# Performance work log

Hardware: AMD Instinct MI355X
Metric: run time of the kernel (lower is better)

Reference implementation:

```python
import jax, jax.numpy as jnp
import numpy as np

IMG_W, IMG_H, STRIDE = 640, 360, 32
S = 72
FMAP_H, FMAP_W = IMG_H // STRIDE, IMG_W // STRIDE  # 11, 20
C_IN, C_AF = 512, 64
B, T = 8, 4
LEFT = [72., 60., 49., 39., 30., 22.]
RIGHT = [108., 120., 131., 141., 150., 158.]
BOTTOM = [165., 150., 141., 131., 120., 108., 100., 90., 80., 72., 60., 49., 39., 30., 15.]


def _side_anchors(angles, nb, ys, x=None, y=None):
    # replicates LaneATT generate_side_anchors / generate_anchor, vectorized
    if x is not None:
        sx = np.full(nb, x, np.float64); sy = np.linspace(1., 0., nb)
    else:
        sx = np.linspace(1., 0., nb); sy = np.full(nb, y, np.float64)
    t = np.tan(np.deg2rad(np.asarray(angles, np.float64)))  # [J]
    # xs[i,j,s] = (sx_i + (1 - ys_s - 1 + sy_i)/tan(angle_j)) * img_w
    xs = (sx[:, None, None] + (1. - ys[None, None, :] - 1. + sy[:, None, None]) / t[None, :, None]) * IMG_W
    n = nb * len(angles)
    A = np.zeros((n, 5 + len(ys)), np.float32)
    A[:, 2] = np.repeat(1. - sy, len(angles))
    A[:, 3] = np.repeat(sx, len(angles))
    A[:, 5:] = xs.reshape(n, len(ys)).astype(np.float32)
    return A


def _gen_anchors(ys):
    left = _side_anchors(LEFT, 72, ys, x=0.)
    right = _side_anchors(RIGHT, 72, ys, x=1.)
    bottom = _side_anchors(BOTTOM, 128, ys, y=1.)
    return np.concatenate([left, bottom, right], axis=0)


def setup_inputs() -> dict:
    key = jax.random.key(0)
    ks = jax.random.split(key, 10)
    anchors = _gen_anchors(np.linspace(1., 0., S))            # [A, 77]
    anchors_cut = _gen_anchors(np.linspace(1., 0., FMAP_H))   # [A, 16]
    A = anchors.shape[0]  # 2784
    # compute_anchor_cut_indices
    unclamped = np.flip(np.round(anchors_cut[:, 5:] / STRIDE), axis=1).astype(np.int32)  # [A, H]
    cut_xs = np.clip(unclamped, 0, FMAP_W - 1)
    invalid_mask = (unclamped < 0) | (unclamped > FMAP_W)
    D = C_AF * FMAP_H  # 704
    head_in = (T + 1) * D  # (time_window_size+1)*anchor_feat_channels*fmap_h = 3520
    inp = {
        'x': jax.random.normal(ks[0], (B, T, C_IN, FMAP_H, FMAP_W), jnp.float32),
        'conv1_w': jax.random.normal(ks[1], (C_AF, C_IN), jnp.float32) * 0.02,
        'conv1_b': jnp.zeros((C_AF,), jnp.float32),
        'att_w': jax.random.normal(ks[2], (D, A - 1), jnp.float32) * 0.001,
        'att_b': jnp.zeros((A - 1,), jnp.float32),
        'cls_w': jax.random.normal(ks[3], (head_in, 2), jnp.float32) * 0.001,
        'cls_b': jnp.zeros((2,), jnp.float32),
        'reg_w': jax.random.normal(ks[4], (head_in, S + 2), jnp.float32) * 0.001,
        'reg_b': jnp.zeros((S + 2,), jnp.float32),
        'anchors': jnp.asarray(anchors),
        'cut_xs': jnp.asarray(cut_xs),
        'invalid_mask': jnp.asarray(invalid_mask),
    }
    return inp


def reference(x, conv1_w, conv1_b, att_w, att_b, cls_w, cls_b, reg_w, reg_b,
              anchors, cut_xs, invalid_mask):
    B_, T_, _, H, W = x.shape
    A = anchors.shape[0]
    # conv1: 1x1 conv over backbone features
    feats = jnp.einsum('btchw,oc->btohw', x, conv1_w) + conv1_b[None, None, :, None, None]
    # cut_anchor_features: gather rois[b,t,c,a,h] = feats[b,t,c,h,cut_xs[a,h]]
    Hy = jnp.broadcast_to(jnp.arange(H), cut_xs.shape)       # [A, H]
    rois = feats[:, :, :, Hy, cut_xs]                        # [B, T, C_af, A, H]
    rois = jnp.where(invalid_mask[None, None, None], 0.0, rois)
    rois = jnp.transpose(rois, (0, 1, 3, 2, 4))              # [B, T, A, C_af, H]
    C_af = rois.shape[3]
    D = C_af * H
    past = rois[:, :-1].reshape(B_, T_ - 1, A, D)            # [B, T-1, A, D]
    cur = rois[:, -1].reshape(B_, A, D)                      # [B, A, D]
    # attention_mechanism: softmax scores scattered into off-diagonal of [A, A]
    scores = cur.reshape(B_ * A, D) @ att_w + att_b          # [B*A, A-1]
    att = jax.nn.softmax(scores, axis=1).reshape(B_, A, A - 1)
    j = jnp.arange(A)
    i = j[:, None]
    # column j of row i maps to source index j - (j>i); diagonal is zero
    k = jnp.minimum(jnp.where(j[None, :] > i, j[None, :] - 1, j[None, :]), A - 2)
    Ibd = jnp.broadcast_to(i, (A, A))
    M = jnp.where(jnp.eye(A, dtype=bool)[None], 0.0, att[:, Ibd, k])  # [B, A, A]
    att_feat = jnp.einsum('bia,bad->bid', M, cur)            # [B, A, D]
    # head input: [past frames | attention features | current frame]
    past_p = jnp.transpose(past, (0, 2, 1, 3)).reshape(B_ * A, (T_ - 1) * D)
    head_in = jnp.concatenate([past_p, att_feat.reshape(B_ * A, D), cur.reshape(B_ * A, D)], axis=1)
    cls = (head_in @ cls_w + cls_b).reshape(B_, A, 2)
    reg = (head_in @ reg_w + reg_b).reshape(B_, A, -1)       # [B, A, n_offsets+2]
    base = jnp.broadcast_to(anchors[None], (B_, A, anchors.shape[1]))
    # reg_proposals: [:, :, :2]=cls ; [:, :, 2] from anchor ; [:, :, 3:] = anchor + reg
    reg_proposals = jnp.concatenate([cls, base[..., 2:3], base[..., 3:] + reg], axis=-1)
    return reg_proposals  # [B, A, 5 + n_offsets]
```

## Files before the change

### kernel.cpp

```cpp
#include <hip/hip_runtime.h>

#define BB 8
#define TT 4
#define CIN 512
#define CAF 64
#define HH 11
#define WW 20
#define PP 220
#define PPAD 256
#define AREAL 2784
#define AP 2816
#define DD 704
#define NH 80
#define NHP 128
#define KH 3520
#define NATT 2783

typedef __attribute__((ext_vector_type(8))) short bf16x8;
typedef __attribute__((ext_vector_type(4))) float floatx4;

__device__ __forceinline__ short f2bf(float f) {
  unsigned u = __float_as_uint(f);
  u += 0x7fffu + ((u >> 16) & 1u);
  return (short)(u >> 16);
}
__device__ __forceinline__ float bf2f(short s) {
  return __uint_as_float(((unsigned)(unsigned short)s) << 16);
}

__device__ __forceinline__ void gload_lds16(const void* g, void* l) {
  __builtin_amdgcn_global_load_lds(
      (const __attribute__((address_space(1))) void*)g,
      (__attribute__((address_space(3))) void*)l, 16, 0, 0);
}

__global__ __launch_bounds__(256)
void transpose_x_kernel(const float* __restrict__ x, short* __restrict__ xT)
{
  int bt = blockIdx.x;
  int c0 = blockIdx.y * 32;
  __shared__ float xs[32 * PP];
  int tid = threadIdx.x;
  const float* xp = x + ((long)bt * CIN + c0) * PP;
  for (int i = tid; i < 32 * PP; i += 256) xs[i] = xp[i];
  __syncthreads();
  short* op = xT + (long)bt * PPAD * CIN + c0;
  for (int j = tid; j < PPAD * 32; j += 256) {
    int p = j >> 5, cc = j & 31;
    short v = 0;
    if (p < PP) v = f2bf(xs[cc * PP + p]);
    op[(long)p * CIN + cc] = v;
  }
}

__global__ void prep_wbf_kernel(const float* __restrict__ w, short* __restrict__ wb)
{
  int idx = blockIdx.x * 256 + threadIdx.x;
  if (idx >= 128 * CIN) return;
  int n = idx >> 9, c = idx & 511;
  wb[idx] = (n < CAF) ? f2bf(w[(long)n * CIN + c]) : (short)0;
}

__global__ __launch_bounds__(256)
void gather_cur_kernel(const short* __restrict__ fpo_base, const int* __restrict__ cut_xs,
                       const int* __restrict__ invalid, short* __restrict__ curR)
{
  int g = blockIdx.y;
  int idx = blockIdx.x * 256 + threadIdx.x;
  int a = idx / 88;
  int ch = idx - a * 88;
  int d0 = ch * 8;
  bf16x8 v = {};
  if (a < AREAL) {
    const short* fp = fpo_base + ((long)g * TT + 3) * PPAD * 128;
    #pragma unroll
    for (int e = 0; e < 8; ++e) {
      int d = d0 + e;
      int o = d / 11;
      int hh = d - o * 11;
      int xw = cut_xs[a * 11 + hh];
      v[e] = invalid[a * 11 + hh] ? (short)0 : fp[(hh * 20 + xw) * 128 + o];
    }
  }
  *(bf16x8*)(curR + ((long)g * AP + a) * DD + d0) = v;
}

__global__ __launch_bounds__(256)
void gather_past_kernel(const short* __restrict__ fpo_base, const int* __restrict__ cut_xs,
                        const int* __restrict__ invalid, short* __restrict__ pastR)
{
  int ty = blockIdx.y;
  int g = ty / 3, t = ty - g * 3;
  int idx = blockIdx.x * 256 + threadIdx.x;
  int a = idx / 88;
  int ch = idx - a * 88;
  int d0 = ch * 8;
  bf16x8 v = {};
  if (a < AREAL) {
    const short* fp = fpo_base + ((long)g * TT + t) * PPAD * 128;
    #pragma unroll
    for (int e = 0; e < 8; ++e) {
      int d = d0 + e;
      int o = d / 11;
      int hh = d - o * 11;
      int xw = cut_xs[a * 11 + hh];
      v[e] = invalid[a * 11 + hh] ? (short)0 : fp[(hh * 20 + xw) * 128 + o];
    }
  }
  *(bf16x8*)(pastR + ((long)ty * AP + a) * DD + d0) = v;
}

__global__ __launch_bounds__(256)
void prep_attw_kernel(const float* __restrict__ att_w, short* __restrict__ attwT)
{
  int n0 = blockIdx.x * 32;
  int d0 = blockIdx.y * 32;
  __shared__ float tile[32][33];
  int tid = threadIdx.x;
  for (int i = tid; i < 1024; i += 256) {
    int r = i >> 5, c = i & 31;
    int d = d0 + r, n = n0 + c;
    tile[r][c] = (d < DD && n < NATT) ? att_w[(long)d * NATT + n] : 0.f;
  }
  __syncthreads();
  for (int i = tid; i < 1024; i += 256) {
    int r = i >> 5, c = i & 31;
    attwT[(long)(n0 + r) * DD + d0 + c] = f2bf(tile[c][r]);
  }
}

__global__ void prep_headw_kernel(const float* __restrict__ cls_w, const float* __restrict__ reg_w,
                                  short* __restrict__ headwT)
{
  long idx = (long)blockIdx.x * 256 + threadIdx.x;
  if (idx >= (long)NHP * KH) return;
  int n = (int)(idx / KH), k = (int)(idx % KH);
  float v = 0.f;
  if (n < 2) v = cls_w[(long)k * 2 + n];
  else if (n < 76) v = reg_w[(long)k * 74 + (n - 2)];
  headwT[idx] = f2bf(v);
}

__global__ __launch_bounds__(512, 2)
void gemm256_nt_kernel(const short* __restrict__ A, long long aBatch, int lda,
                       const short* __restrict__ Bt, long long bBatch, int ldb,
                       short* __restrict__ C, long long cBatch, int ldc,
                       int K, const float* __restrict__ bias, int biasN)
{
  int gx = gridDim.x, gy = gridDim.y;
  int nwg = gx * gy * gridDim.z;
  int o = blockIdx.x + gx * (blockIdx.y + gy * blockIdx.z);
  int xcd = o & 7, pos = o >> 3;
  int q = nwg >> 3, r = nwg & 7;
  int nid = (xcd < r ? xcd * (q + 1) : r * (q + 1) + (xcd - r) * q) + pos;
  int bx = nid % gx; int tq = nid / gx; int by = tq % gy; int bz = tq / gy;

  A  += (long long)bz * aBatch;
  Bt += (long long)bz * bBatch;
  C  += (long long)bz * cBatch;
  int M0 = by * 256, N0 = bx * 256;

  __shared__ short lds_a[2 * 256 * 64];
  __shared__ short lds_b[2 * 256 * 64];

  int tid = threadIdx.x, lane = tid & 63, w = tid >> 6;
  int wr = w >> 2, wc = w & 3;

  floatx4 acc[8][4];
  #pragma unroll
  for (int m = 0; m < 8; ++m)
    #pragma unroll
    for (int n = 0; n < 4; ++n) acc[m][n] = floatx4{0.f, 0.f, 0.f, 0.f};

  int rl = tid >> 3, sl = tid & 7;
  int ssl = sl ^ (rl & 7);
  const short* aS = A  + (long)(M0 + rl) * lda + ssl * 8;
  const short* bS = Bt + (long)(N0 + rl) * ldb + ssl * 8;
  char* la0 = (char*)lds_a;
  char* lb0 = (char*)lds_b;
  int wub = (tid & ~63) * 16;

  auto stage = [&](int kt, int buf) {
    long ko = (long)kt * 64;
    #pragma unroll
    for (int c = 0; c < 4; ++c) {
      gload_lds16(aS + (long)c * 64 * lda + ko, la0 + buf * 32768 + c * 8192 + wub);
      gload_lds16(bS + (long)c * 64 * ldb + ko, lb0 + buf * 32768 + c * 8192 + wub);
    }
  };
  auto rdA = [&](int buf, int mf, int kk) -> bf16x8 {
    int row = wr * 128 + mf * 16 + (lane & 15);
    int phys = (kk * 4 + (lane >> 4)) ^ (lane & 7);
    return *(const bf16x8*)(la0 + buf * 32768 + row * 128 + phys * 16);
  };
  auto rdB = [&](int buf, int nf, int kk) -> bf16x8 {
    int row = wc * 64 + nf * 16 + (lane & 15);
    int phys = (kk * 4 + (lane >> 4)) ^ (lane & 7);
    return *(const bf16x8*)(lb0 + buf * 32768 + row * 128 + phys * 16);
  };

  int nt = K >> 6;
  stage(0, 0);
  stage(1, 1);
  asm volatile("s_waitcnt vmcnt(8)" ::: "memory");
  __builtin_amdgcn_sched_barrier(0);
  __builtin_amdgcn_s_barrier();
  __builtin_amdgcn_sched_barrier(0);

  for (int t = 0; t < nt; ++t) {
    int buf = t & 1;
    bf16x8 A0[2][4], A1[2][4], B0[2][2], B1[2][2];
    #pragma unroll
    for (int kk = 0; kk < 2; ++kk) {
      #pragma unroll
      for (int i = 0; i < 4; ++i) A0[kk][i] = rdA(buf, i, kk);
      #pragma unroll
      for (int j = 0; j < 2; ++j) B0[kk][j] = rdB(buf, j, kk);
    }
    __builtin_amdgcn_s_setprio(1);
    #pragma unroll
    for (int kk = 0; kk < 2; ++kk)
      #pragma unroll
      for (int i = 0; i < 4; ++i)
        #pragma unroll
        for (int j = 0; j < 2; ++j)
          acc[i][j] = __builtin_amdgcn_mfma_f32_16x16x32_bf16(A0[kk][i], B0[kk][j], acc[i][j], 0, 0, 0);
    __builtin_amdgcn_s_setprio(0);
    #pragma unroll
    for (int kk = 0; kk < 2; ++kk)
      #pragma unroll
      for (int j = 0; j < 2; ++j) B1[kk][j] = rdB(buf, 2 + j, kk);
    __builtin_amdgcn_s_setprio(1);
    #pragma unroll
    for (int kk = 0; kk < 2; ++kk)
      #pragma unroll
      for (int i = 0; i < 4; ++i)
        #pragma unroll
        for (int j = 0; j < 2; ++j)
          acc[i][2 + j] = __builtin_amdgcn_mfma_f32_16x16x32_bf16(A0[kk][i], B1[kk][j], acc[i][2 + j], 0, 0, 0);
    __builtin_amdgcn_s_setprio(0);
    #pragma unroll
    for (int kk = 0; kk < 2; ++kk)
      #pragma unroll
      for (int i = 0; i < 4; ++i) A1[kk][i] = rdA(buf, 4 + i, kk);
    __builtin_amdgcn_s_setprio(1);
    #pragma unroll
    for (int kk = 0; kk < 2; ++kk)
      #pragma unroll
      for (int i = 0; i < 4; ++i)
        #pragma unroll
        for (int j = 0; j < 2; ++j)
          acc[4 + i][2 + j] = __builtin_amdgcn_mfma_f32_16x16x32_bf16(A1[kk][i], B1[kk][j], acc[4 + i][2 + j], 0, 0, 0);
    __builtin_amdgcn_s_setprio(0);
    __builtin_amdgcn_sched_barrier(0);
    __builtin_amdgcn_s_barrier();
    __builtin_amdgcn_sched_barrier(0);
    if (t + 2 < nt) stage(t + 2, buf);
    __builtin_amdgcn_s_setprio(1);
    #pragma unroll
    for (int kk = 0; kk < 2; ++kk)
      #pragma unroll
      for (int i = 0; i < 4; ++i)
        #pragma unroll
        for (int j = 0; j < 2; ++j)
          acc[4 + i][j] = __builtin_amdgcn_mfma_f32_16x16x32_bf16(A1[kk][i], B0[kk][j], acc[4 + i][j], 0, 0, 0);
    __builtin_amdgcn_s_setprio(0);
    if (t + 2 < nt) {
      asm volatile("s_waitcnt vmcnt(8)" ::: "memory");
    } else {
      asm volatile("s_waitcnt vmcnt(0)" ::: "memory");
    }
    __builtin_amdgcn_sched_barrier(0);
    __builtin_amdgcn_s_barrier();
    __builtin_amdgcn_sched_barrier(0);
  }

  #pragma unroll
  for (int mf = 0; mf < 8; ++mf) {
    #pragma unroll
    for (int nf = 0; nf < 4; ++nf) {
      int col = N0 + wc * 64 + nf * 16 + (lane & 15);
      float bv = 0.f;
      if (bias) bv = (col < biasN) ? bias[col] : 0.f;
      #pragma unroll
      for (int rr = 0; rr < 4; ++rr) {
        int rowc = M0 + wr * 128 + mf * 16 + (lane >> 4) * 4 + rr;
        C[(long)rowc * ldc + col] = f2bf(acc[mf][nf][rr] + bv);
      }
    }
  }
}

template<int WITH_BIAS>
__global__ __launch_bounds__(256)
void gemm_nt_kernel(const short* __restrict__ A, long long aBatch, int lda,
                    const short* __restrict__ Bt, long long bBatch, int ldb,
                    short* __restrict__ C, long long cBatch, int ldc,
                    int K, const float* __restrict__ bias, int biasN)
{
  int gx = gridDim.x, gy = gridDim.y;
  int nwg = gx * gy * gridDim.z;
  int o = blockIdx.x + gx * (blockIdx.y + gy * blockIdx.z);
  int xcd = o & 7, pos = o >> 3;
  int q = nwg >> 3, r = nwg & 7;
  int nid = (xcd < r ? xcd * (q + 1) : r * (q + 1) + (xcd - r) * q) + pos;
  int bx = nid % gx; int t = nid / gx; int by = t % gy; int bz = t / gy;

  A  += (long long)bz * aBatch;
  Bt += (long long)bz * bBatch;
  C  += (long long)bz * cBatch;
  int m0 = by * 128;
  int n0 = bx * 128;

  __shared__ short lds_a[2 * 128 * 32];
  __shared__ short lds_b[2 * 128 * 32];

  int tid = threadIdx.x;
  int lane = tid & 63;
  int wid = tid >> 6;
  int wr = wid >> 1, wc = wid & 1;
  int row = tid >> 2;
  int slot = tid & 3;

  floatx4 acc[4][4];
  #pragma unroll
  for (int m = 0; m < 4; ++m)
    #pragma unroll
    for (int n = 0; n < 4; ++n) acc[m][n] = floatx4{0.f, 0.f, 0.f, 0.f};

  int wbase = (tid & ~63) * 16;
  int ks0 = slot ^ ((row >> 1) & 3);
  int ks1 = slot ^ (((row + 64) >> 1) & 3);
  const short* ar0 = A  + (long)(m0 + row) * lda + ks0 * 8;
  const short* ar1 = A  + (long)(m0 + row + 64) * lda + ks1 * 8;
  const short* br0 = Bt + (long)(n0 + row) * ldb + ks0 * 8;
  const short* br1 = Bt + (long)(n0 + row + 64) * ldb + ks1 * 8;

  auto stage = [&](int kt, int buf) {
    int k0 = kt * 32;
    char* la = (char*)lds_a + buf * 8192 + wbase;
    char* lb = (char*)lds_b + buf * 8192 + wbase;
    gload_lds16(ar0 + k0, la);
    gload_lds16(ar1 + k0, la + 4096);
    gload_lds16(br0 + k0, lb);
    gload_lds16(br1 + k0, lb + 4096);
  };

  int nk = K >> 5;
  stage(0, 0);
  __syncthreads();
  int cur = 0;
  for (int kt = 0; kt < nk; ++kt) {
    if (kt + 1 < nk) stage(kt + 1, cur ^ 1);
    const char* ba = (const char*)lds_a + cur * 8192;
    const char* bb = (const char*)lds_b + cur * 8192;
    bf16x8 af[4], bfv[4];
    #pragma unroll
    for (int m = 0; m < 4; ++m) {
      int rw = wr * 64 + m * 16 + (lane & 15);
      int pp = (lane >> 4) ^ ((rw >> 1) & 3);
      af[m] = *(const bf16x8*)(ba + rw * 64 + (pp << 4));
    }
    #pragma unroll
    for (int n = 0; n < 4; ++n) {
      int rw = wc * 64 + n * 16 + (lane & 15);
      int pp = (lane >> 4) ^ ((rw >> 1) & 3);
      bfv[n] = *(const bf16x8*)(bb + rw * 64 + (pp << 4));
    }
    #pragma unroll
    for (int m = 0; m < 4; ++m)
      #pragma unroll
      for (int n = 0; n < 4; ++n)
        acc[m][n] = __builtin_amdgcn_mfma_f32_16x16x32_bf16(af[m], bfv[n], acc[m][n], 0, 0, 0);
    __syncthreads();
    cur ^= 1;
  }

  #pragma unroll
  for (int m = 0; m < 4; ++m) {
    #pragma unroll
    for (int n = 0; n < 4; ++n) {
      int col = n0 + wc * 64 + n * 16 + (lane & 15);
      float bv = 0.f;
      if (WITH_BIAS) bv = (col < biasN) ? bias[col] : 0.f;
      #pragma unroll
      for (int rr = 0; rr < 4; ++rr) {
        int rowc = m0 + wr * 64 + m * 16 + (lane >> 4) * 4 + rr;
        C[(long)rowc * ldc + col] = f2bf(acc[m][n][rr] + bv);
      }
    }
  }
}

__global__ __launch_bounds__(256)
void softmax_shift_kernel(short* __restrict__ scores)
{
  int g = blockIdx.y;
  int i = blockIdx.x;
  short* row = scores + (long)g * AP * AP + (long)i * AP;
  __shared__ float vals[NATT];
  __shared__ float red[4];
  int tid = threadIdx.x;

  float lmax = -1e30f;
  for (int jc = tid; jc < 348; jc += 256) {
    bf16x8 v8 = *(const bf16x8*)(row + jc * 8);
    #pragma unroll
    for (int e = 0; e < 8; ++e) {
      int j = jc * 8 + e;
      float f = bf2f(v8[e]);
      if (j < NATT) { vals[j] = f; lmax = fmaxf(lmax, f); }
    }
  }
  #pragma unroll
  for (int off = 32; off; off >>= 1) lmax = fmaxf(lmax, __shfl_down(lmax, off, 64));
  if ((tid & 63) == 0) red[tid >> 6] = lmax;
  __syncthreads();
  float mx = fmaxf(fmaxf(red[0], red[1]), fmaxf(red[2], red[3]));
  __syncthreads();

  float lsum = 0.f;
  for (int j = tid; j < NATT; j += 256) {
    float e = __expf(vals[j] - mx);
    vals[j] = e;
    lsum += e;
  }
  #pragma unroll
  for (int off = 32; off; off >>= 1) lsum += __shfl_down(lsum, off, 64);
  if ((tid & 63) == 0) red[tid >> 6] = lsum;
  __syncthreads();
  float inv = 1.f / (red[0] + red[1] + red[2] + red[3]);
  __syncthreads();

  for (int jc = tid; jc < 352; jc += 256) {
    bf16x8 o8;
    #pragma unroll
    for (int e = 0; e < 8; ++e) {
      int j = jc * 8 + e;
      float v;
      if (j < i)            v = vals[j] * inv;
      else if (j == i)      v = 0.f;
      else if (j < AREAL)   v = vals[j - 1] * inv;
      else                  v = 0.f;
      o8[e] = f2bf(v);
    }
    *(bf16x8*)(row + jc * 8) = o8;
  }
}

__device__ __forceinline__
void gemm_n80_body(const short* __restrict__ abase, int ald, int m0,
                   const short* __restrict__ hb, int ldbh,
                   short* __restrict__ lp, int nk,
                   short* lds_a, short* lds_b)
{
  int tid = threadIdx.x, lane = tid & 63, wid = tid >> 6;

  floatx4 acc[2][5];
  #pragma unroll
  for (int m = 0; m < 2; ++m)
    #pragma unroll
    for (int n = 0; n < 5; ++n) acc[m][n] = floatx4{0.f, 0.f, 0.f, 0.f};

  bf16x8 ra[2], rb0, rb1, xa[2], xb0, xb1;
  bool has2 = (tid < 64);

  auto stage_load = [&](int kt, bf16x8* r_a, bf16x8& r_b0, bf16x8& r_b1) {
    int kk = kt * 32;
    #pragma unroll
    for (int it = 0; it < 2; ++it) {
      int rw = it * 64 + (tid >> 2);
      int ks = (tid & 3) ^ ((rw >> 1) & 3);
      r_a[it] = *(const bf16x8*)(abase + (long)(m0 + rw) * ald + kk + ks * 8);
    }
    {
      int n = tid >> 2;
      int ks = (tid & 3) ^ ((n >> 1) & 3);
      r_b0 = *(const bf16x8*)(hb + (long)n * ldbh + kk + ks * 8);
    }
    if (has2) {
      int n = (tid + 256) >> 2;
      int ks = (tid & 3) ^ ((n >> 1) & 3);
      r_b1 = *(const bf16x8*)(hb + (long)n * ldbh + kk + ks * 8);
    }
  };
  auto stage_write = [&](int buf, bf16x8* r_a, bf16x8& r_b0, bf16x8& r_b1) {
    char* la = (char*)lds_a + buf * 8192;
    char* lb = (char*)lds_b + buf * 8192;
    #pragma unroll
    for (int it = 0; it < 2; ++it) {
      int rw = it * 64 + (tid >> 2);
      *(bf16x8*)(la + rw * 64 + ((tid & 3) << 4)) = r_a[it];
    }
    { int n = tid >> 2;
      *(bf16x8*)(lb + n * 64 + ((tid & 3) << 4)) = r_b0; }
    if (has2) {
      int n = (tid + 256) >> 2;
      *(bf16x8*)(lb + n * 64 + ((tid & 3) << 4)) = r_b1;
    }
  };

  stage_load(0, ra, rb0, rb1);
  stage_write(0, ra, rb0, rb1);
  __syncthreads();
  int cur = 0;
  for (int kt = 0; kt < nk; ++kt) {
    bool more = (kt + 1 < nk);
    if (more) stage_load(kt + 1, xa, xb0, xb1);
    const char* la = (const char*)lds_a + cur * 8192;
    const char* lb = (const char*)lds_b + cur * 8192;
    bf16x8 af[2], bfv[5];
    #pragma unroll
    for (int m = 0; m < 2; ++m) {
      int rw = wid * 32 + m * 16 + (lane & 15);
      int pp = (lane >> 4) ^ ((rw >> 1) & 3);
      af[m] = *(const bf16x8*)(la + rw * 64 + (pp << 4));
    }
    #pragma unroll
    for (int n = 0; n < 5; ++n) {
      int nn = n * 16 + (lane & 15);
      int pp = (lane >> 4) ^ ((nn >> 1) & 3);
      bfv[n] = *(const bf16x8*)(lb + nn * 64 + (pp << 4));
    }
    #pragma unroll
    for (int m = 0; m < 2; ++m)
      #pragma unroll
      for (int n = 0; n < 5; ++n)
        acc[m][n] = __builtin_amdgcn_mfma_f32_16x16x32_bf16(af[m], bfv[n], acc[m][n], 0, 0, 0);
    if (more) stage_write(cur ^ 1, xa, xb0, xb1);
    __syncthreads();
    cur ^= 1;
  }

  #pragma unroll
  for (int fm = 0; fm < 2; ++fm)
    #pragma unroll
    for (int fn = 0; fn < 5; ++fn)
      #pragma unroll
      for (int rr = 0; rr < 4; ++rr) {
        int rw = m0 + wid * 32 + fm * 16 + (lane >> 4) * 4 + rr;
        int col = fn * 16 + (lane & 15);
        lp[(long)rw * NH + col] = f2bf(acc[fm][fn][rr]);
      }
}

__global__ __launch_bounds__(256)
void gemm_heads_kernel(const short* __restrict__ pastR, const short* __restrict__ curR,
                       const short* __restrict__ headwT, short* __restrict__ linpart, int G)
{
  int kc = blockIdx.x;
  int m0 = blockIdx.y * 128;
  int g  = blockIdx.z;
  const short* abase;
  const short* hb;
  if (kc == 3) { abase = curR + (long)g * AP * DD; hb = headwT + 4 * DD; }
  else         { abase = pastR + (long)(g * 3 + kc) * AP * DD; hb = headwT + kc * DD; }
  __shared__ short lds_a[2 * 128 * 32];
  __shared__ short lds_b[2 * 128 * 32];
  short* lp = linpart + (long)(kc * G + g) * AP * NH;
  gemm_n80_body(abase, DD, m0, hb, KH, lp, DD / 32, lds_a, lds_b);
}

__global__ __launch_bounds__(256)
void gemm_skinny_kernel(const short* __restrict__ scores, const short* __restrict__ curW3T,
                        short* __restrict__ linpart, int G)
{
  int kc = blockIdx.x;
  int m0 = blockIdx.y * 128;
  int g  = blockIdx.z;
  const short* abase = scores + (long)g * AP * AP + (long)kc * 704;
  const short* hb    = curW3T + (long)g * NHP * AP + (long)kc * 704;
  __shared__ short lds_a[2 * 128 * 32];
  __shared__ short lds_b[2 * 128 * 32];
  short* lp = linpart + (long)((4 + kc) * G + g) * AP * NH;
  gemm_n80_body(abase, AP, m0, hb, AP, lp, 704 / 32, lds_a, lds_b);
}

__global__ void assemble_kernel(const short* __restrict__ linpart, const float* __restrict__ anchors,
                                const float* __restrict__ cls_b, const float* __restrict__ reg_b,
                                float* __restrict__ out_b0, int G)
{
  long idx = (long)blockIdx.x * 256 + threadIdx.x;
  const long per_g = (long)AREAL * 77;
  if (idx >= per_g * G) return;
  int g = (int)(idx / per_g);
  long rem = idx - (long)g * per_g;
  int c = (int)(rem % 77);
  int a = (int)(rem / 77);
  float v;
  if (c == 2) {
    v = anchors[(long)a * 77 + 2];
  } else {
    int col = (c < 2) ? c : (2 + (c - 3));
    float s = 0.f;
    #pragma unroll
    for (int sl = 0; sl < 8; ++sl)
      s += bf2f(linpart[((long)(sl * G + g) * AP + a) * NH + col]);
    v = (c < 2) ? (s + cls_b[c]) : (anchors[(long)a * 77 + c] + s + reg_b[c - 3]);
  }
  out_b0[idx] = v;
}

extern "C" void kernel_launch(void* const* d_in, const int* in_sizes, int n_in,
                              void* d_out, int out_size, void* d_ws, size_t ws_size,
                              hipStream_t stream)
{
  (void)in_sizes; (void)n_in; (void)out_size;
  const float* x        = (const float*)d_in[0];
  const float* conv1_w  = (const float*)d_in[1];
  const float* conv1_b  = (const float*)d_in[2];
  const float* att_w    = (const float*)d_in[3];
  const float* att_b    = (const float*)d_in[4];
  const float* cls_w    = (const float*)d_in[5];
  const float* cls_b    = (const float*)d_in[6];
  const float* reg_w    = (const float*)d_in[7];
  const float* reg_b    = (const float*)d_in[8];
  const float* anchors  = (const float*)d_in[9];
  const int*   cut_xs   = (const int*)d_in[10];
  const int*   invalid  = (const int*)d_in[11];
  float* out = (float*)d_out;

  auto align256 = [](size_t v) { return (v + 255) & ~(size_t)255; };
  const size_t sz_feats  = align256((size_t)BB * TT * PPAD * 128 * 2);
  const size_t sz_wbf    = align256((size_t)128 * CIN * 2);
  const size_t sz_attwT  = align256((size_t)AP * DD * 2);
  const size_t sz_headwT = align256((size_t)NHP * KH * 2);
  const size_t misc = sz_feats + sz_wbf + sz_attwT + sz_headwT;
  auto per_g = [&](int G) {
    return align256((size_t)G * AP * DD * 2)
         + align256((size_t)G * AP * AP * 2)
         + align256((size_t)G * NHP * AP * 2)
         + align256((size_t)8 * G * AP * NH * 2);
  };
  int G = 1;
  for (int cand : {8, 4, 2}) {
    if (misc + per_g(cand) + (1u << 20) <= ws_size) { G = cand; break; }
  }

  char* p = (char*)d_ws;
  short* feats_po = (short*)p; p += sz_feats;
  short* w_bf16   = (short*)p; p += sz_wbf;
  short* attwT    = (short*)p; p += sz_attwT;
  short* headwT   = (short*)p; p += sz_headwT;
  short* curR     = (short*)p; p += align256((size_t)G * AP * DD * 2);
  short* scores   = (short*)p; p += align256((size_t)G * AP * AP * 2);
  short* curW3T   = (short*)p; p += align256((size_t)G * NHP * AP * 2);
  short* linpart  = (short*)p; p += align256((size_t)8 * G * AP * NH * 2);
  short* xT       = scores;
  short* pastR    = scores;

  transpose_x_kernel<<<dim3(BB * TT, CIN / 32), 256, 0, stream>>>(x, xT);
  prep_wbf_kernel<<<(128 * CIN + 255) / 256, 256, 0, stream>>>(conv1_w, w_bf16);
  prep_attw_kernel<<<dim3(AP / 32, DD / 32), 256, 0, stream>>>(att_w, attwT);
  prep_headw_kernel<<<(NHP * KH + 255) / 256, 256, 0, stream>>>(cls_w, reg_w, headwT);

  gemm_nt_kernel<1><<<dim3(1, BB * TT * PPAD / 128, 1), 256, 0, stream>>>(
      xT, 0, CIN, w_bf16, 0, CIN, feats_po, 0, 128, CIN, conv1_b, CAF);

  for (int b0 = 0; b0 < BB; b0 += G) {
    const short* fpo = feats_po + (long)b0 * TT * PPAD * 128;

    gather_cur_kernel<<<dim3(AP * 88 / 256, G), 256, 0, stream>>>(fpo, cut_xs, invalid, curR);

    gemm256_nt_kernel<<<dim3(AP / 256, G * AP / 256, 1), 512, 0, stream>>>(
        curR, 0, DD, attwT, 0, DD, scores, 0, AP, DD, att_b, NATT);

    softmax_shift_kernel<<<dim3(AREAL, G), 256, 0, stream>>>(scores);

    gemm_nt_kernel<0><<<dim3(AP / 128, 1, G), 256, 0, stream>>>(
        headwT + 3 * DD, 0, KH, curR, (long long)AP * DD, DD,
        curW3T, (long long)NHP * AP, AP, DD, nullptr, 0);

    gemm_skinny_kernel<<<dim3(4, AP / 128, G), 256, 0, stream>>>(scores, curW3T, linpart, G);

    gather_past_kernel<<<dim3(AP * 88 / 256, 3 * G), 256, 0, stream>>>(fpo, cut_xs, invalid, pastR);

    gemm_heads_kernel<<<dim3(4, AP / 128, G), 256, 0, stream>>>(pastR, curR, headwT, linpart, G);

    assemble_kernel<<<(int)(((long)G * AREAL * 77 + 255) / 256), 256, 0, stream>>>(
        linpart, anchors, cls_b, reg_b, out + (long)b0 * AREAL * 77, G);
  }
}
```

Measured before the change: 391.1 us.

## Fuse past-frame gather into head GEMM and merge tail GEMMs into one launch

Precomputes a combined gather index table (cut x plus invalid flag) once, so each gathered element needs one index load instead of two. The past-frame gather kernel is removed: the head GEMM now gathers past-frame features straight from the feature map into its A-tile loads, which avoids writing and re-reading the pastR buffer. The skinny attention GEMM and the head GEMMs are merged into a single 8-way launch. In exchange, the fused GEMM does scattered per-element gathers on its A-load path, which may stall the pipeline, and different blocks within one launch now run different code paths.

```diff
diff --git a/kernel.cpp b/kernel.cpp
--- a/kernel.cpp
+++ b/kernel.cpp
@@ -61,9 +61,18 @@
   wb[idx] = (n < CAF) ? f2bf(w[(long)n * CIN + c]) : (short)0;
 }
 
+__global__ void prep_gidx_kernel(const int* __restrict__ cut_xs, const int* __restrict__ invalid,
+                                 int* __restrict__ gidx)
+{
+  int idx = blockIdx.x * 256 + threadIdx.x;
+  if (idx >= AREAL * HH) return;
+  int hh = idx % HH;
+  gidx[idx] = invalid[idx] ? -1 : (hh * WW + cut_xs[idx]) * 128;
+}
+
 __global__ __launch_bounds__(256)
-void gather_cur_kernel(const short* __restrict__ fpo_base, const int* __restrict__ cut_xs,
-                       const int* __restrict__ invalid, short* __restrict__ curR)
+void gather_cur_kernel(const short* __restrict__ fpo_base, const int* __restrict__ gidx,
+                       short* __restrict__ curR)
 {
   int g = blockIdx.y;
   int idx = blockIdx.x * 256 + threadIdx.x;
@@ -78,36 +87,11 @@
       int d = d0 + e;
       int o = d / 11;
       int hh = d - o * 11;
-      int xw = cut_xs[a * 11 + hh];
-      v[e] = invalid[a * 11 + hh] ? (short)0 : fp[(hh * 20 + xw) * 128 + o];
+      int gi = gidx[a * 11 + hh];
+      v[e] = (gi < 0) ? (short)0 : fp[gi + o];
     }
   }
   *(bf16x8*)(curR + ((long)g * AP + a) * DD + d0) = v;
-}
-
-__global__ __launch_bounds__(256)
-void gather_past_kernel(const short* __restrict__ fpo_base, const int* __restrict__ cut_xs,
-                        const int* __restrict__ invalid, short* __restrict__ pastR)
-{
-  int ty = blockIdx.y;
-  int g = ty / 3, t = ty - g * 3;
-  int idx = blockIdx.x * 256 + threadIdx.x;
-  int a = idx / 88;
-  int ch = idx - a * 88;
-  int d0 = ch * 8;
-  bf16x8 v = {};
-  if (a < AREAL) {
-    const short* fp = fpo_base + ((long)g * TT + t) * PPAD * 128;
-    #pragma unroll
-    for (int e = 0; e < 8; ++e) {
-      int d = d0 + e;
-      int o = d / 11;
-      int hh = d - o * 11;
-      int xw = cut_xs[a * 11 + hh];
-      v[e] = invalid[a * 11 + hh] ? (short)0 : fp[(hh * 20 + xw) * 128 + o];
-    }
-  }
-  *(bf16x8*)(pastR + ((long)ty * AP + a) * DD + d0) = v;
 }
 
 __global__ __launch_bounds__(256)
@@ -544,36 +528,141 @@
       }
 }
 
+__device__ __forceinline__
+void gemm_n80_gather_body(const short* __restrict__ fp, const int* __restrict__ gidx,
+                          int m0, const short* __restrict__ hb,
+                          short* __restrict__ lp,
+                          short* lds_a, short* lds_b)
+{
+  int tid = threadIdx.x, lane = tid & 63, wid = tid >> 6;
+
+  floatx4 acc[2][5];
+  #pragma unroll
+  for (int m = 0; m < 2; ++m)
+    #pragma unroll
+    for (int n = 0; n < 5; ++n) acc[m][n] = floatx4{0.f, 0.f, 0.f, 0.f};
+
+  bf16x8 ra[2], rb0, rb1, xa[2], xb0, xb1;
+  bool has2 = (tid < 64);
+
+  auto stage_load = [&](int kt, bf16x8* r_a, bf16x8& r_b0, bf16x8& r_b1) {
+    #pragma unroll
+    for (int it = 0; it < 2; ++it) {
+      int rw = it * 64 + (tid >> 2);
+      int a = m0 + rw;
+      int ks = (tid & 3) ^ ((rw >> 1) & 3);
+      int d0 = kt * 32 + ks * 8;
+      bf16x8 v = {};
+      if (a < AREAL) {
+        #pragma unroll
+        for (int e = 0; e < 8; ++e) {
+          int d = d0 + e;
+          int o = d / 11;
+          int hh = d - o * 11;
+          int gi = gidx[a * 11 + hh];
+          v[e] = (gi < 0) ? (short)0 : fp[gi + o];
+        }
+      }
+      r_a[it] = v;
+    }
+    int kk = kt * 32;
+    {
+      int n = tid >> 2;
+      int ks = (tid & 3) ^ ((n >> 1) & 3);
+      r_b0 = *(const bf16x8*)(hb + (long)n * KH + kk + ks * 8);
+    }
+    if (has2) {
+      int n = (tid + 256) >> 2;
+      int ks = (tid & 3) ^ ((n >> 1) & 3);
+      r_b1 = *(const bf16x8*)(hb + (long)n * KH + kk + ks * 8);
+    }
+  };
+  auto stage_write = [&](int buf, bf16x8* r_a, bf16x8& r_b0, bf16x8& r_b1) {
+    char* la = (char*)lds_a + buf * 8192;
+    char* lb = (char*)lds_b + buf * 8192;
+    #pragma unroll
+    for (int it = 0; it < 2; ++it) {
+      int rw = it * 64 + (tid >> 2);
+      *(bf16x8*)(la + rw * 64 + ((tid & 3) << 4)) = r_a[it];
+    }
+    { int n = tid >> 2;
+      *(bf16x8*)(lb + n * 64 + ((tid & 3) << 4)) = r_b0; }
+    if (has2) {
+      int n = (tid + 256) >> 2;
+      *(bf16x8*)(lb + n * 64 + ((tid & 3) << 4)) = r_b1;
+    }
+  };
+
+  const int nk = 22;
+  stage_load(0, ra, rb0, rb1);
+  stage_write(0, ra, rb0, rb1);
+  __syncthreads();
+  int cur = 0;
+  for (int kt = 0; kt < nk; ++kt) {
+    bool more = (kt + 1 < nk);
+    if (more) stage_load(kt + 1, xa, xb0, xb1);
+    const char* la = (const char*)lds_a + cur * 8192;
+    const char* lb = (const char*)lds_b + cur * 8192;
+    bf16x8 af[2], bfv[5];
+    #pragma unroll
+    for (int m = 0; m < 2; ++m) {
+      int rw = wid * 32 + m * 16 + (lane & 15);
+      int pp = (lane >> 4) ^ ((rw >> 1) & 3);
+      af[m] = *(const bf16x8*)(la + rw * 64 + (pp << 4));
+    }
+    #pragma unroll
+    for (int n = 0; n < 5; ++n) {
+      int nn = n * 16 + (lane & 15);
+      int pp = (lane >> 4) ^ ((nn >> 1) & 3);
+      bfv[n] = *(const bf16x8*)(lb + nn * 64 + (pp << 4));
+    }
+    #pragma unroll
+    for (int m = 0; m < 2; ++m)
+      #pragma unroll
+      for (int n = 0; n < 5; ++n)
+        acc[m][n] = __builtin_amdgcn_mfma_f32_16x16x32_bf16(af[m], bfv[n], acc[m][n], 0, 0, 0);
+    if (more) stage_write(cur ^ 1, xa, xb0, xb1);
+    __syncthreads();
+    cur ^= 1;
+  }
+
+  #pragma unroll
+  for (int fm = 0; fm < 2; ++fm)
+    #pragma unroll
+    for (int fn = 0; fn < 5; ++fn)
+      #pragma unroll
+      for (int rr = 0; rr < 4; ++rr) {
+        int rw = m0 + wid * 32 + fm * 16 + (lane >> 4) * 4 + rr;
+        int col = fn * 16 + (lane & 15);
+        lp[(long)rw * NH + col] = f2bf(acc[fm][fn][rr]);
+      }
+}
+
 __global__ __launch_bounds__(256)
-void gemm_heads_kernel(const short* __restrict__ pastR, const short* __restrict__ curR,
-                       const short* __restrict__ headwT, short* __restrict__ linpart, int G)
+void gemm_tail_kernel(const short* __restrict__ fpo_base, const int* __restrict__ gidx,
+                      const short* __restrict__ curR, const short* __restrict__ scores,
+                      const short* __restrict__ curW3T, const short* __restrict__ headwT,
+                      short* __restrict__ linpart, int G)
 {
   int kc = blockIdx.x;
   int m0 = blockIdx.y * 128;
   int g  = blockIdx.z;
-  const short* abase;
-  const short* hb;
-  if (kc == 3) { abase = curR + (long)g * AP * DD; hb = headwT + 4 * DD; }
-  else         { abase = pastR + (long)(g * 3 + kc) * AP * DD; hb = headwT + kc * DD; }
   __shared__ short lds_a[2 * 128 * 32];
   __shared__ short lds_b[2 * 128 * 32];
   short* lp = linpart + (long)(kc * G + g) * AP * NH;
-  gemm_n80_body(abase, DD, m0, hb, KH, lp, DD / 32, lds_a, lds_b);
-}
-
-__global__ __launch_bounds__(256)
-void gemm_skinny_kernel(const short* __restrict__ scores, const short* __restrict__ curW3T,
-                        short* __restrict__ linpart, int G)
-{
-  int kc = blockIdx.x;
-  int m0 = blockIdx.y * 128;
-  int g  = blockIdx.z;
-  const short* abase = scores + (long)g * AP * AP + (long)kc * 704;
-  const short* hb    = curW3T + (long)g * NHP * AP + (long)kc * 704;
-  __shared__ short lds_a[2 * 128 * 32];
-  __shared__ short lds_b[2 * 128 * 32];
-  short* lp = linpart + (long)((4 + kc) * G + g) * AP * NH;
-  gemm_n80_body(abase, AP, m0, hb, AP, lp, 704 / 32, lds_a, lds_b);
+
+  if (kc < 3) {
+    const short* fp = fpo_base + ((long)g * TT + kc) * PPAD * 128;
+    gemm_n80_gather_body(fp, gidx, m0, headwT + kc * DD, lp, lds_a, lds_b);
+  } else if (kc == 3) {
+    gemm_n80_body(curR + (long)g * AP * DD, DD, m0, headwT + 4 * DD, KH, lp,
+                  DD / 32, lds_a, lds_b);
+  } else {
+    int c = kc - 4;
+    gemm_n80_body(scores + (long)g * AP * AP + (long)c * 704, AP, m0,
+                  curW3T + (long)g * NHP * AP + (long)c * 704, AP, lp,
+                  704 / 32, lds_a, lds_b);
+  }
 }
 
 __global__ void assemble_kernel(const short* __restrict__ linpart, const float* __restrict__ anchors,
@@ -625,7 +714,8 @@
   const size_t sz_wbf    = align256((size_t)128 * CIN * 2);
   const size_t sz_attwT  = align256((size_t)AP * DD * 2);
   const size_t sz_headwT = align256((size_t)NHP * KH * 2);
-  const size_t misc = sz_feats + sz_wbf + sz_attwT + sz_headwT;
+  const size_t sz_gidx   = align256((size_t)AREAL * HH * 4);
+  const size_t misc = sz_feats + sz_wbf + sz_attwT + sz_headwT + sz_gidx;
   auto per_g = [&](int G) {
     return align256((size_t)G * AP * DD * 2)
          + align256((size_t)G * AP * AP * 2)
@@ -642,17 +732,18 @@
   short* w_bf16   = (short*)p; p += sz_wbf;
   short* attwT    = (short*)p; p += sz_attwT;
   short* headwT   = (short*)p; p += sz_headwT;
+  int*   gidx     = (int*)p;   p += sz_gidx;
   short* curR     = (short*)p; p += align256((size_t)G * AP * DD * 2);
   short* scores   = (short*)p; p += align256((size_t)G * AP * AP * 2);
   short* curW3T   = (short*)p; p += align256((size_t)G * NHP * AP * 2);
   short* linpart  = (short*)p; p += align256((size_t)8 * G * AP * NH * 2);
   short* xT       = scores;
-  short* pastR    = scores;
 
   transpose_x_kernel<<<dim3(BB * TT, CIN / 32), 256, 0, stream>>>(x, xT);
   prep_wbf_kernel<<<(128 * CIN + 255) / 256, 256, 0, stream>>>(conv1_w, w_bf16);
   prep_attw_kernel<<<dim3(AP / 32, DD / 32), 256, 0, stream>>>(att_w, attwT);
   prep_headw_kernel<<<(NHP * KH + 255) / 256, 256, 0, stream>>>(cls_w, reg_w, headwT);
+  prep_gidx_kernel<<<(AREAL * HH + 255) / 256, 256, 0, stream>>>(cut_xs, invalid, gidx);
 
   gemm_nt_kernel<1><<<dim3(1, BB * TT * PPAD / 128, 1), 256, 0, stream>>>(
       xT, 0, CIN, w_bf16, 0, CIN, feats_po, 0, 128, CIN, conv1_b, CAF);
@@ -660,7 +751,7 @@
   for (int b0 = 0; b0 < BB; b0 += G) {
     const short* fpo = feats_po + (long)b0 * TT * PPAD * 128;
 
-    gather_cur_kernel<<<dim3(AP * 88 / 256, G), 256, 0, stream>>>(fpo, cut_xs, invalid, curR);
+    gather_cur_kernel<<<dim3(AP * 88 / 256, G), 256, 0, stream>>>(fpo, gidx, curR);
 
     gemm256_nt_kernel<<<dim3(AP / 256, G * AP / 256, 1), 512, 0, stream>>>(
         curR, 0, DD, attwT, 0, DD, scores, 0, AP, DD, att_b, NATT);
@@ -671,11 +762,8 @@
         headwT + 3 * DD, 0, KH, curR, (long long)AP * DD, DD,
         curW3T, (long long)NHP * AP, AP, DD, nullptr, 0);
 
-    gemm_skinny_kernel<<<dim3(4, AP / 128, G), 256, 0, stream>>>(scores, curW3T, linpart, G);
-
-    gather_past_kernel<<<dim3(AP * 88 / 256, 3 * G), 256, 0, stream>>>(fpo, cut_xs, invalid, pastR);
-
-    gemm_heads_kernel<<<dim3(4, AP / 128, G), 256, 0, stream>>>(pastR, curR, headwT, linpart, G);
+    gemm_tail_kernel<<<dim3(8, AP / 128, G), 256, 0, stream>>>(
+        fpo, gidx, curR, scores, curW3T, headwT, linpart, G);
 
     assemble_kernel<<<(int)(((long)G * AREAL * 77 + 255) / 256), 256, 0, stream>>>(
         linpart, anchors, cls_b, reg_b, out + (long)b0 * AREAL * 77, G);
```

Measured after the change: 465.9 us. 19.1% more time.

## Precompute gather indices and use direct global-to-LDS loads in n80 GEMM

Applied to the files above, without the earlier changes.

Adds a prep kernel that folds cut_xs and the invalid mask into one precomputed offset table, so the gather kernels do one int load per element instead of two. It also rewrites the staging in the N=80 GEMM body to use gload_lds16, which copies global memory straight into LDS instead of staging through registers. The aim is fewer register-staged memory operations and a lower VGPR count in the heads GEMMs. The direct-to-LDS path changes the LDS placement to per-wave linear slots, and it relies on the swizzle still matching the existing fragment reads. The N tile is 80 wide but row+64 loads cover 128 rows of B, so it reads the padded headwT rows.

```diff
diff --git a/kernel.cpp b/kernel.cpp
--- a/kernel.cpp
+++ b/kernel.cpp
@@ -61,9 +61,18 @@
   wb[idx] = (n < CAF) ? f2bf(w[(long)n * CIN + c]) : (short)0;
 }
 
-__global__ __launch_bounds__(256)
-void gather_cur_kernel(const short* __restrict__ fpo_base, const int* __restrict__ cut_xs,
-                       const int* __restrict__ invalid, short* __restrict__ curR)
+__global__ void prep_gidx_kernel(const int* __restrict__ cut_xs, const int* __restrict__ invalid,
+                                 int* __restrict__ gidx)
+{
+  int idx = blockIdx.x * 256 + threadIdx.x;
+  if (idx >= AREAL * HH) return;
+  int hh = idx % HH;
+  gidx[idx] = invalid[idx] ? -1 : (hh * WW + cut_xs[idx]) * 128;
+}
+
+__global__ __launch_bounds__(256)
+void gather_cur_kernel(const short* __restrict__ fpo_base, const int* __restrict__ gidx,
+                       short* __restrict__ curR)
 {
   int g = blockIdx.y;
   int idx = blockIdx.x * 256 + threadIdx.x;
@@ -78,16 +87,16 @@
       int d = d0 + e;
       int o = d / 11;
       int hh = d - o * 11;
-      int xw = cut_xs[a * 11 + hh];
-      v[e] = invalid[a * 11 + hh] ? (short)0 : fp[(hh * 20 + xw) * 128 + o];
+      int gi = gidx[a * 11 + hh];
+      v[e] = (gi < 0) ? (short)0 : fp[gi + o];
     }
   }
   *(bf16x8*)(curR + ((long)g * AP + a) * DD + d0) = v;
 }
 
 __global__ __launch_bounds__(256)
-void gather_past_kernel(const short* __restrict__ fpo_base, const int* __restrict__ cut_xs,
-                        const int* __restrict__ invalid, short* __restrict__ pastR)
+void gather_past_kernel(const short* __restrict__ fpo_base, const int* __restrict__ gidx,
+                        short* __restrict__ pastR)
 {
   int ty = blockIdx.y;
   int g = ty / 3, t = ty - g * 3;
@@ -103,8 +112,8 @@
       int d = d0 + e;
       int o = d / 11;
       int hh = d - o * 11;
-      int xw = cut_xs[a * 11 + hh];
-      v[e] = invalid[a * 11 + hh] ? (short)0 : fp[(hh * 20 + xw) * 128 + o];
+      int gi = gidx[a * 11 + hh];
+      v[e] = (gi < 0) ? (short)0 : fp[gi + o];
     }
   }
   *(bf16x8*)(pastR + ((long)ty * AP + a) * DD + d0) = v;
@@ -462,51 +471,31 @@
     #pragma unroll
     for (int n = 0; n < 5; ++n) acc[m][n] = floatx4{0.f, 0.f, 0.f, 0.f};
 
-  bf16x8 ra[2], rb0, rb1, xa[2], xb0, xb1;
-  bool has2 = (tid < 64);
-
-  auto stage_load = [&](int kt, bf16x8* r_a, bf16x8& r_b0, bf16x8& r_b1) {
-    int kk = kt * 32;
-    #pragma unroll
-    for (int it = 0; it < 2; ++it) {
-      int rw = it * 64 + (tid >> 2);
-      int ks = (tid & 3) ^ ((rw >> 1) & 3);
-      r_a[it] = *(const bf16x8*)(abase + (long)(m0 + rw) * ald + kk + ks * 8);
-    }
-    {
-      int n = tid >> 2;
-      int ks = (tid & 3) ^ ((n >> 1) & 3);
-      r_b0 = *(const bf16x8*)(hb + (long)n * ldbh + kk + ks * 8);
-    }
-    if (has2) {
-      int n = (tid + 256) >> 2;
-      int ks = (tid & 3) ^ ((n >> 1) & 3);
-      r_b1 = *(const bf16x8*)(hb + (long)n * ldbh + kk + ks * 8);
-    }
+  int wbase = (tid & ~63) * 16;
+  int row = tid >> 2;
+  int slot = tid & 3;
+  int ks0 = slot ^ ((row >> 1) & 3);
+  int ks1 = slot ^ (((row + 64) >> 1) & 3);
+  const short* ar0 = abase + (long)(m0 + row) * ald + ks0 * 8;
+  const short* ar1 = abase + (long)(m0 + row + 64) * ald + ks1 * 8;
+  const short* br0 = hb + (long)row * ldbh + ks0 * 8;
+  const short* br1 = hb + (long)(row + 64) * ldbh + ks1 * 8;
+
+  auto stage = [&](int kt, int buf) {
+    int k0 = kt * 32;
+    char* la = (char*)lds_a + buf * 8192 + wbase;
+    char* lb = (char*)lds_b + buf * 8192 + wbase;
+    gload_lds16(ar0 + k0, la);
+    gload_lds16(ar1 + k0, la + 4096);
+    gload_lds16(br0 + k0, lb);
+    gload_lds16(br1 + k0, lb + 4096);
   };
-  auto stage_write = [&](int buf, bf16x8* r_a, bf16x8& r_b0, bf16x8& r_b1) {
-    char* la = (char*)lds_a + buf * 8192;
-    char* lb = (char*)lds_b + buf * 8192;
-    #pragma unroll
-    for (int it = 0; it < 2; ++it) {
-      int rw = it * 64 + (tid >> 2);
-      *(bf16x8*)(la + rw * 64 + ((tid & 3) << 4)) = r_a[it];
-    }
-    { int n = tid >> 2;
-      *(bf16x8*)(lb + n * 64 + ((tid & 3) << 4)) = r_b0; }
-    if (has2) {
-      int n = (tid + 256) >> 2;
-      *(bf16x8*)(lb + n * 64 + ((tid & 3) << 4)) = r_b1;
-    }
-  };
-
-  stage_load(0, ra, rb0, rb1);
-  stage_write(0, ra, rb0, rb1);
+
+  stage(0, 0);
   __syncthreads();
   int cur = 0;
   for (int kt = 0; kt < nk; ++kt) {
-    bool more = (kt + 1 < nk);
-    if (more) stage_load(kt + 1, xa, xb0, xb1);
+    if (kt + 1 < nk) stage(kt + 1, cur ^ 1);
     const char* la = (const char*)lds_a + cur * 8192;
     const char* lb = (const char*)lds_b + cur * 8192;
     bf16x8 af[2], bfv[5];
@@ -527,7 +516,6 @@
       #pragma unroll
       for (int n = 0; n < 5; ++n)
         acc[m][n] = __builtin_amdgcn_mfma_f32_16x16x32_bf16(af[m], bfv[n], acc[m][n], 0, 0, 0);
-    if (more) stage_write(cur ^ 1, xa, xb0, xb1);
     __syncthreads();
     cur ^= 1;
   }
@@ -625,7 +613,8 @@
   const size_t sz_wbf    = align256((size_t)128 * CIN * 2);
   const size_t sz_attwT  = align256((size_t)AP * DD * 2);
   const size_t sz_headwT = align256((size_t)NHP * KH * 2);
-  const size_t misc = sz_feats + sz_wbf + sz_attwT + sz_headwT;
+  const size_t sz_gidx   = align256((size_t)AREAL * HH * 4);
+  const size_t misc = sz_feats + sz_wbf + sz_attwT + sz_headwT + sz_gidx;
   auto per_g = [&](int G) {
     return align256((size_t)G * AP * DD * 2)
          + align256((size_t)G * AP * AP * 2)
@@ -642,6 +631,7 @@
   short* w_bf16   = (short*)p; p += sz_wbf;
   short* attwT    = (short*)p; p += sz_attwT;
   short* headwT   = (short*)p; p += sz_headwT;
+  int*   gidx     = (int*)p;   p += sz_gidx;
   short* curR     = (short*)p; p += align256((size_t)G * AP * DD * 2);
   short* scores   = (short*)p; p += align256((size_t)G * AP * AP * 2);
   short* curW3T   = (short*)p; p += align256((size_t)G * NHP * AP * 2);
@@ -653,6 +643,7 @@
   prep_wbf_kernel<<<(128 * CIN + 255) / 256, 256, 0, stream>>>(conv1_w, w_bf16);
   prep_attw_kernel<<<dim3(AP / 32, DD / 32), 256, 0, stream>>>(att_w, attwT);
   prep_headw_kernel<<<(NHP * KH + 255) / 256, 256, 0, stream>>>(cls_w, reg_w, headwT);
+  prep_gidx_kernel<<<(AREAL * HH + 255) / 256, 256, 0, stream>>>(cut_xs, invalid, gidx);
 
   gemm_nt_kernel<1><<<dim3(1, BB * TT * PPAD / 128, 1), 256, 0, stream>>>(
       xT, 0, CIN, w_bf16, 0, CIN, feats_po, 0, 128, CIN, conv1_b, CAF);
@@ -660,7 +651,7 @@
   for (int b0 = 0; b0 < BB; b0 += G) {
     const short* fpo = feats_po + (long)b0 * TT * PPAD * 128;
 
-    gather_cur_kernel<<<dim3(AP * 88 / 256, G), 256, 0, stream>>>(fpo, cut_xs, invalid, curR);
+    gather_cur_kernel<<<dim3(AP * 88 / 256, G), 256, 0, stream>>>(fpo, gidx, curR);
 
     gemm256_nt_kernel<<<dim3(AP / 256, G * AP / 256, 1), 512, 0, stream>>>(
         curR, 0, DD, attwT, 0, DD, scores, 0, AP, DD, att_b, NATT);
@@ -673,7 +664,7 @@
 
     gemm_skinny_kernel<<<dim3(4, AP / 128, G), 256, 0, stream>>>(scores, curW3T, linpart, G);
 
-    gather_past_kernel<<<dim3(AP * 88 / 256, 3 * G), 256, 0, stream>>>(fpo, cut_xs, invalid, pastR);
+    gather_past_kernel<<<dim3(AP * 88 / 256, 3 * G), 256, 0, stream>>>(fpo, gidx, pastR);
 
     gemm_heads_kernel<<<dim3(4, AP / 128, G), 256, 0, stream>>>(pastR, curR, headwT, linpart, G);
 
```

Result: faster. 379.6 us (-2.9%).
